# Kernel tuning notes

Hardware: AMD Instinct MI355X
Metric: run time of the kernel (lower is better)

The kernel has to match this reference:

```python
import jax, jax.numpy as jnp
import numpy as np

K = 1024   # codebook size
C = 8      # codebook channels
D = K // C # per-channel code dim = 128
BETA = 0.25
B = 8192   # batch of latent vectors, each of size C*D = K


def setup_inputs() -> dict:
    key = jax.random.key(0)
    k1, k2, k3 = jax.random.split(key, 3)
    latents = jax.random.normal(k1, (B, C * D), dtype=jnp.float32)
    # nn.Embedding(K, D) init: uniform(-1/K, 1/K)
    embedding = jax.random.uniform(k2, (K, D), dtype=jnp.float32,
                                   minval=-1.0 / K, maxval=1.0 / K)
    k = jax.random.randint(k3, (C,), 0, 8, dtype=jnp.int32)
    return {"latents": latents, "embedding": embedding, "k": k}


def reference(latents, embedding, k):
    sg = jax.lax.stop_gradient
    flat = latents.reshape(-1, D)                                  # [B*C, D]
    # squared euclidean distance to every code: [B*C, K]
    dist = (jnp.sum(flat ** 2, axis=1, keepdims=True)
            + jnp.sum(embedding ** 2, axis=1)
            - 2.0 * (flat @ embedding.T))
    order = jnp.argsort(dist, axis=1).reshape(-1, C, K)            # [B, C, K]
    # per channel c, pick the k[c]-th nearest code index
    sel = jnp.take_along_axis(order, k[None, :, None], axis=2)[..., 0]  # [B, C]
    # one-hot @ embedding == plain gather of selected rows
    quantized = embedding[sel.reshape(-1)].reshape(latents.shape)  # [B, C*D]
    commitment_loss = jnp.mean((sg(quantized) - latents) ** 2)
    embedding_loss = jnp.mean((quantized - sg(latents)) ** 2)
    vq_loss = BETA * commitment_loss + embedding_loss
    # straight-through estimator
    quantized_st = latents + sg(quantized - latents)
    return quantized_st, vq_loss
```

## Files before the change

### kernel.cpp

```cpp
#include <hip/hip_runtime.h>

#define KDIM   128
#define BM     128
#define NELEM  8388608

#define OFF_ESQ   36864
#define OFF_EBUF0 40960
#define OFF_FSQ   57344
#define OFF_SEL   57856
#define OFF_RED   58368
#define SMEM_SZ   58400

typedef __attribute__((ext_vector_type(8)))  short  short8;
typedef __attribute__((ext_vector_type(8)))  __bf16 bf16x8;
typedef __attribute__((ext_vector_type(4)))  float  f32x4;

__device__ inline ushort f2bf(float f) {
  unsigned u = __builtin_bit_cast(unsigned, f);
  u += 0x7fffu + ((u >> 16) & 1u);
  return (ushort)(u >> 16);
}
__device__ inline f32x4 mfma16(short8 a, short8 b, f32x4 c) {
  return __builtin_amdgcn_mfma_f32_16x16x32_bf16(
      __builtin_bit_cast(bf16x8, a), __builtin_bit_cast(bf16x8, b), c, 0, 0, 0);
}
__device__ inline void gload16(const void* g, void* l) {
  __builtin_amdgcn_global_load_lds(
      (const __attribute__((address_space(1))) unsigned*)g,
      (__attribute__((address_space(3))) unsigned*)l, 16, 0, 0);
}

__global__ void vq_prep(const float* __restrict__ emb, ushort* __restrict__ ebf,
                        float* __restrict__ esqm) {
  int j = blockIdx.x, d = threadIdx.x;
  float v = emb[j * KDIM + d];
  ebf[j * KDIM + (d ^ ((j & 7) << 3))] = f2bf(v);
  float s = v * v;
#pragma unroll
  for (int m = 1; m <= 32; m <<= 1) s += __shfl_xor(s, m);
  __shared__ float w[2];
  if ((threadIdx.x & 63) == 0) w[threadIdx.x >> 6] = s;
  __syncthreads();
  if (threadIdx.x == 0) esqm[j] = -0.5f * (w[0] + w[1]);
}

__global__ __launch_bounds__(256, 2) void vq_main(
    const float* __restrict__ lat, const float* __restrict__ emb,
    const int* __restrict__ ksel, const ushort* __restrict__ ebf,
    const float* __restrict__ esqm, float* __restrict__ out,
    float* __restrict__ partial) {
  __shared__ __align__(16) unsigned char smem[SMEM_SZ];
  ushort* fLds    = (ushort*)(smem);
  float*  mbuf    = (float*)(smem);
  float*  esqmLds = (float*)(smem + OFF_ESQ);
  float*  fsqLds  = (float*)(smem + OFF_FSQ);
  int*    selLds  = (int*)(smem + OFF_SEL);
  float*  redL    = (float*)(smem + OFF_RED);

  const int tid = threadIdx.x;
  const int lane = tid & 63, wid = tid >> 6;
  const int gR0 = blockIdx.x * BM;

  {
    const char* src = (const char*)ebf + tid * 16;
    char* dst = (char*)smem + OFF_EBUF0 + tid * 16;
#pragma unroll
    for (int q = 0; q < 4; ++q) gload16(src + q * 4096, dst + q * 4096);
  }
  ((float4*)esqmLds)[tid] = ((const float4*)esqm)[tid];

#pragma unroll
  for (int it = 0; it < 16; ++it) {
    int i = tid + it * 256;
    int row = i >> 5, c4 = i & 31;
    float4 v = *(const float4*)(lat + (size_t)(gR0 + row) * KDIM + c4 * 4);
    float s = v.x * v.x + v.y * v.y + v.z * v.z + v.w * v.w;
#pragma unroll
    for (int m = 1; m <= 16; m <<= 1) s += __shfl_xor(s, m);
    if ((i & 31) == 0) fsqLds[row] = s;
    ushort4 b; b.x = f2bf(v.x); b.y = f2bf(v.y); b.z = f2bf(v.z); b.w = f2bf(v.w);
    *(ushort4*)(&fLds[row * 144 + c4 * 4]) = b;
  }
  __syncthreads();

  const int n = lane & 15, hi = lane >> 4;
  const int g = wid >> 1, h = wid & 1;
  short8 bfr[4][4];
#pragma unroll
  for (int ct = 0; ct < 4; ++ct)
#pragma unroll
    for (int s = 0; s < 4; ++s)
      bfr[ct][s] = *(const short8*)(&fLds[(g * 64 + ct * 16 + n) * 144 + s * 32 + hi * 8]);
  asm volatile("s_waitcnt lgkmcnt(0)" ::: "memory");

  const int pb = ((hi ^ (n & 3)) << 4) | (((n >> 2) & 1) << 6);
  const int rowb = h * 8192 + n * 256;
  const char* aE0 = (const char*)smem + OFF_EBUF0 + rowb + pb;
  const char* aO0 = (const char*)smem + OFF_EBUF0 + rowb + (pb ^ 64);
  const char* aE1 = (const char*)smem + 0 + rowb + pb;
  const char* aO1 = (const char*)smem + 0 + rowb + (pb ^ 64);

  int cst[2][4];
#pragma unroll
  for (int t = 0; t < 2; ++t)
#pragma unroll
    for (int r = 0; r < 4; ++r) cst[t][r] = h * 32 + t * 16 + hi * 4 + r;

  const float NINF = __builtin_bit_cast(float, 0xFF800000u);
  float top[4][8];
#pragma unroll
  for (int ct = 0; ct < 4; ++ct)
#pragma unroll
    for (int p = 0; p < 8; ++p) top[ct][p] = NINF;

#pragma unroll 2
  for (int nn = 0; nn < 16; ++nn) {
    __builtin_amdgcn_s_barrier();
    if (nn < 15) {
      const char* src = (const char*)ebf + (nn + 1) * 16384 + tid * 16;
      char* dst = (char*)smem + ((nn & 1) ? OFF_EBUF0 : 0) + tid * 16;
#pragma unroll
      for (int q = 0; q < 4; ++q) gload16(src + q * 4096, dst + q * 4096);
      asm volatile("s_waitcnt vmcnt(4)" ::: "memory");
    } else {
      asm volatile("s_waitcnt vmcnt(0)" ::: "memory");
    }
    __builtin_amdgcn_s_barrier();

    const char* aEb = (nn & 1) ? aE1 : aE0;
    const char* aOb = (nn & 1) ? aO1 : aO0;

    f32x4 acc[2][4];
#pragma unroll
    for (int t = 0; t < 2; ++t) {
      f32x4 e = *(const f32x4*)(esqmLds + nn * 64 + h * 32 + t * 16 + hi * 4);
#pragma unroll
      for (int ct = 0; ct < 4; ++ct) acc[t][ct] = e;
    }
#pragma unroll
    for (int s = 0; s < 4; ++s) {
      const char* ab = (s & 1) ? aOb : aEb;
      const int so = (s >> 1) * 128;
      short8 a0 = *(const short8*)(ab + so);
      short8 a1 = *(const short8*)(ab + 4096 + so);
#pragma unroll
      for (int ct = 0; ct < 4; ++ct) {
        acc[0][ct] = mfma16(a0, bfr[ct][s], acc[0][ct]);
        acc[1][ct] = mfma16(a1, bfr[ct][s], acc[1][ct]);
      }
    }

#pragma unroll
    for (int ct = 0; ct < 4; ++ct) {
      float k[8];
#pragma unroll
      for (int t = 0; t < 2; ++t)
#pragma unroll
        for (int r = 0; r < 4; ++r) {
          unsigned bb = (__builtin_bit_cast(unsigned, acc[t][ct][r]) & 0xFFFFFC00u)
                        | (unsigned)cst[t][r];
          k[t * 4 + r] = __builtin_bit_cast(float, bb);
        }
      float x = fmaxf(fmaxf(k[0], k[1]), k[2]);
      float y = fmaxf(fmaxf(k[3], k[4]), k[5]);
      float c = fmaxf(fmaxf(x, y), fmaxf(k[6], k[7]));
      unsigned cb = __builtin_bit_cast(unsigned, c) | (unsigned)(nn << 6);
      float key = __builtin_bit_cast(float, cb);
#pragma unroll
      for (int p = 0; p < 8; ++p) {
        float mx = fmaxf(top[ct][p], key);
        key = fminf(top[ct][p], key);
        top[ct][p] = mx;
      }
    }
  }

  __syncthreads();

#pragma unroll
  for (int ct = 0; ct < 4; ++ct) {
    const int L = g * 64 + ct * 16 + n;
    const int sl = (h * 4 + hi) ^ (n & 7);
    float* dst = mbuf + L * 68 + sl * 8;
    *(f32x4*)(dst + 0) = (f32x4){top[ct][0], top[ct][1], top[ct][2], top[ct][3]};
    *(f32x4*)(dst + 4) = (f32x4){top[ct][4], top[ct][5], top[ct][6], top[ct][7]};
  }
  __syncthreads();

  if (tid < 128) {
    const int L = tid, xk = L & 7;
    int kk = ksel[L & 7]; kk = kk < 0 ? 0 : (kk > 7 ? 7 : kk);
    float hh[8]; int ix[8];
#pragma unroll
    for (int j = 0; j < 8; ++j) { hh[j] = mbuf[L * 68 + ((j ^ xk) << 3)]; ix[j] = 0; }
    float sel;
    for (int s = 0;; ++s) {
      float m01 = fmaxf(fmaxf(hh[0], hh[1]), fmaxf(hh[2], hh[3]));
      float m23 = fmaxf(fmaxf(hh[4], hh[5]), fmaxf(hh[6], hh[7]));
      sel = fmaxf(m01, m23);
      if (s == kk) break;
#pragma unroll
      for (int j = 0; j < 8; ++j) {
        if (hh[j] == sel) {
          ++ix[j];
          hh[j] = (ix[j] < 8) ? mbuf[L * 68 + ((j ^ xk) << 3) + ix[j]] : NINF;
        }
      }
    }
    unsigned sb = __builtin_bit_cast(unsigned, sel);
    selLds[L] = (int)(sb & 1023u);
    float val = __builtin_bit_cast(float, sb & 0xFFFFFC00u);
    float rl = fsqLds[L] - 2.0f * val;
#pragma unroll
    for (int m = 1; m <= 32; m <<= 1) rl += __shfl_xor(rl, m);
    if (lane == 0) redL[wid] = rl;
  }
  __syncthreads();
  if (tid == 0) partial[blockIdx.x] = redL[0] + redL[1];

#pragma unroll
  for (int it = 0; it < 16; ++it) {
    int i = tid + it * 256;
    int row = i >> 5, c4 = i & 31;
    int s2 = selLds[row];
    float4 q = *(const float4*)(emb + (size_t)s2 * KDIM + c4 * 4);
    *(float4*)(out + (size_t)(gR0 + row) * KDIM + c4 * 4) = q;
  }
}

__global__ void vq_reduce(const float* __restrict__ p, float* __restrict__ loss) {
  int t = threadIdx.x;
  double s = (double)p[t] + (double)p[t + 256];
#pragma unroll
  for (int m = 1; m <= 32; m <<= 1) s += __shfl_xor(s, m);
  __shared__ double w[4];
  if ((t & 63) == 0) w[t >> 6] = s;
  __syncthreads();
  if (t == 0) loss[0] = (float)((w[0] + w[1] + w[2] + w[3]) * (1.25 / 8388608.0));
}

extern "C" void kernel_launch(void* const* d_in, const int* in_sizes, int n_in,
                              void* d_out, int out_size, void* d_ws, size_t ws_size,
                              hipStream_t stream) {
  const float* lat = (const float*)d_in[0];
  const float* emb = (const float*)d_in[1];
  const int* ksel = (const int*)d_in[2];
  float* out = (float*)d_out;

  ushort* ebf = (ushort*)d_ws;
  float* esqm = (float*)((char*)d_ws + 262144);
  float* partial = (float*)((char*)d_ws + 266240);

  vq_prep<<<1024, 128, 0, stream>>>(emb, ebf, esqm);
  vq_main<<<512, 256, 0, stream>>>(lat, emb, ksel, ebf, esqm, out, partial);
  vq_reduce<<<1, 256, 0, stream>>>(partial, out + NELEM);
}
```

Measured before the change: 45.95 us.

## Restructure VQ main loop: per-wave rows, larger codebook chunks, register latent fragments

Each wave now owns 32 latent rows and scans the whole codebook, rather than two waves splitting columns for 64 rows. Latents are loaded straight from global memory into bf16 MFMA fragments, with no LDS staging pass. The codebook streams in 32KB double-buffered chunks over 8 iterations, with one barrier per chunk. Per-thread top-8 candidates now come from 4 column slots instead of 8, which shrinks the final merge. LDS use rises to about 70KB, which may reduce occupancy, and each codebook A fragment is reused across only 2 row tiles instead of 4.

```diff
diff --git a/kernel.cpp b/kernel.cpp
--- a/kernel.cpp
+++ b/kernel.cpp
@@ -1,15 +1,14 @@
 #include <hip/hip_runtime.h>
 
 #define KDIM   128
-#define BM     128
 #define NELEM  8388608
 
-#define OFF_ESQ   36864
-#define OFF_EBUF0 40960
-#define OFF_FSQ   57344
-#define OFF_SEL   57856
-#define OFF_RED   58368
-#define SMEM_SZ   58400
+#define OFF_EBUF 0
+#define OFF_ESQ  65536
+#define OFF_FSQ  69632
+#define OFF_SEL  70144
+#define OFF_RED  70656
+#define SMEM_SZ  70688
 
 typedef __attribute__((ext_vector_type(8)))  short  short8;
 typedef __attribute__((ext_vector_type(8)))  __bf16 bf16x8;
@@ -50,160 +49,156 @@
     const float* __restrict__ esqm, float* __restrict__ out,
     float* __restrict__ partial) {
   __shared__ __align__(16) unsigned char smem[SMEM_SZ];
-  ushort* fLds    = (ushort*)(smem);
-  float*  mbuf    = (float*)(smem);
-  float*  esqmLds = (float*)(smem + OFF_ESQ);
-  float*  fsqLds  = (float*)(smem + OFF_FSQ);
-  int*    selLds  = (int*)(smem + OFF_SEL);
-  float*  redL    = (float*)(smem + OFF_RED);
+  float* esqmLds = (float*)(smem + OFF_ESQ);
+  float* fsqLds  = (float*)(smem + OFF_FSQ);
+  int*   selLds  = (int*)(smem + OFF_SEL);
+  float* redL    = (float*)(smem + OFF_RED);
+  float* mbuf    = (float*)(smem + OFF_EBUF);
 
   const int tid = threadIdx.x;
   const int lane = tid & 63, wid = tid >> 6;
-  const int gR0 = blockIdx.x * BM;
+  const int gR0 = blockIdx.x * 128;
+  const int n = lane & 15, hi = lane >> 4;
 
   {
     const char* src = (const char*)ebf + tid * 16;
-    char* dst = (char*)smem + OFF_EBUF0 + tid * 16;
-#pragma unroll
-    for (int q = 0; q < 4; ++q) gload16(src + q * 4096, dst + q * 4096);
+    char* dst = (char*)smem + OFF_EBUF + tid * 16;
+#pragma unroll
+    for (int q = 0; q < 8; ++q) gload16(src + q * 4096, dst + q * 4096);
   }
   ((float4*)esqmLds)[tid] = ((const float4*)esqm)[tid];
 
-#pragma unroll
-  for (int it = 0; it < 16; ++it) {
-    int i = tid + it * 256;
-    int row = i >> 5, c4 = i & 31;
-    float4 v = *(const float4*)(lat + (size_t)(gR0 + row) * KDIM + c4 * 4);
-    float s = v.x * v.x + v.y * v.y + v.z * v.z + v.w * v.w;
-#pragma unroll
-    for (int m = 1; m <= 16; m <<= 1) s += __shfl_xor(s, m);
-    if ((i & 31) == 0) fsqLds[row] = s;
-    ushort4 b; b.x = f2bf(v.x); b.y = f2bf(v.y); b.z = f2bf(v.z); b.w = f2bf(v.w);
-    *(ushort4*)(&fLds[row * 144 + c4 * 4]) = b;
-  }
-  __syncthreads();
-
-  const int n = lane & 15, hi = lane >> 4;
-  const int g = wid >> 1, h = wid & 1;
-  short8 bfr[4][4];
-#pragma unroll
-  for (int ct = 0; ct < 4; ++ct)
-#pragma unroll
-    for (int s = 0; s < 4; ++s)
-      bfr[ct][s] = *(const short8*)(&fLds[(g * 64 + ct * 16 + n) * 144 + s * 32 + hi * 8]);
-  asm volatile("s_waitcnt lgkmcnt(0)" ::: "memory");
-
-  const int pb = ((hi ^ (n & 3)) << 4) | (((n >> 2) & 1) << 6);
-  const int rowb = h * 8192 + n * 256;
-  const char* aE0 = (const char*)smem + OFF_EBUF0 + rowb + pb;
-  const char* aO0 = (const char*)smem + OFF_EBUF0 + rowb + (pb ^ 64);
-  const char* aE1 = (const char*)smem + 0 + rowb + pb;
-  const char* aO1 = (const char*)smem + 0 + rowb + (pb ^ 64);
-
-  int cst[2][4];
-#pragma unroll
-  for (int t = 0; t < 2; ++t)
-#pragma unroll
-    for (int r = 0; r < 4; ++r) cst[t][r] = h * 32 + t * 16 + hi * 4 + r;
+  short8 bfr[2][4];
+  float fsqp[2];
+#pragma unroll
+  for (int ct = 0; ct < 2; ++ct) {
+    const float* rp = lat + (size_t)(gR0 + wid * 32 + ct * 16 + n) * KDIM + hi * 8;
+    float s = 0.f;
+#pragma unroll
+    for (int sfr = 0; sfr < 4; ++sfr) {
+      float4 v0 = *(const float4*)(rp + sfr * 32);
+      float4 v1 = *(const float4*)(rp + sfr * 32 + 4);
+      s += v0.x * v0.x + v0.y * v0.y + v0.z * v0.z + v0.w * v0.w
+         + v1.x * v1.x + v1.y * v1.y + v1.z * v1.z + v1.w * v1.w;
+      short8 b;
+      b[0] = (short)f2bf(v0.x); b[1] = (short)f2bf(v0.y);
+      b[2] = (short)f2bf(v0.z); b[3] = (short)f2bf(v0.w);
+      b[4] = (short)f2bf(v1.x); b[5] = (short)f2bf(v1.y);
+      b[6] = (short)f2bf(v1.z); b[7] = (short)f2bf(v1.w);
+      bfr[ct][sfr] = b;
+    }
+    fsqp[ct] = s;
+  }
+#pragma unroll
+  for (int ct = 0; ct < 2; ++ct) {
+    float s = fsqp[ct];
+    s += __shfl_xor(s, 16);
+    s += __shfl_xor(s, 32);
+    if (hi == 0) fsqLds[wid * 32 + ct * 16 + n] = s;
+  }
+  asm volatile("s_waitcnt vmcnt(0)" ::: "memory");
+  __syncthreads();
+
+  const int nm = n & 7;
+  const int pb = ((hi ^ (nm & 3)) << 4) | (((nm >> 2) & 1) << 6);
+  const char* aE0 = (const char*)smem + OFF_EBUF + n * 256 + pb;
+  const char* aO0 = (const char*)smem + OFF_EBUF + n * 256 + (pb ^ 64);
+
+  int cidx[4];
+#pragma unroll
+  for (int r = 0; r < 4; ++r) cidx[r] = hi * 4 + r;
 
   const float NINF = __builtin_bit_cast(float, 0xFF800000u);
-  float top[4][8];
-#pragma unroll
-  for (int ct = 0; ct < 4; ++ct)
+  float top[2][8];
+#pragma unroll
+  for (int ct = 0; ct < 2; ++ct)
 #pragma unroll
     for (int p = 0; p < 8; ++p) top[ct][p] = NINF;
+  float kq[2][4];
 
 #pragma unroll 2
-  for (int nn = 0; nn < 16; ++nn) {
-    __builtin_amdgcn_s_barrier();
-    if (nn < 15) {
-      const char* src = (const char*)ebf + (nn + 1) * 16384 + tid * 16;
-      char* dst = (char*)smem + ((nn & 1) ? OFF_EBUF0 : 0) + tid * 16;
-#pragma unroll
-      for (int q = 0; q < 4; ++q) gload16(src + q * 4096, dst + q * 4096);
-      asm volatile("s_waitcnt vmcnt(4)" ::: "memory");
-    } else {
+  for (int nn = 0; nn < 8; ++nn) {
+    const int cb = (nn & 1) * 32768;
+    if (nn < 7) {
+      const char* src = (const char*)ebf + (nn + 1) * 32768 + tid * 16;
+      char* dst = (char*)smem + OFF_EBUF + (((nn + 1) & 1) * 32768) + tid * 16;
+#pragma unroll
+      for (int q = 0; q < 8; ++q) gload16(src + q * 4096, dst + q * 4096);
+    }
+    const float* eqb = esqmLds + nn * 128 + hi * 4;
+#pragma unroll
+    for (int tp = 0; tp < 8; ++tp) {
+      f32x4 e = *(const f32x4*)(eqb + tp * 16);
+      f32x4 acc0 = e, acc1 = e;
+#pragma unroll
+      for (int s = 0; s < 4; ++s) {
+        const char* ab = ((s & 1) ? aO0 : aE0) + cb + tp * 4096 + (s >> 1) * 128;
+        short8 a = *(const short8*)ab;
+        acc0 = mfma16(a, bfr[0][s], acc0);
+        acc1 = mfma16(a, bfr[1][s], acc1);
+      }
+      float kn[2][4];
+#pragma unroll
+      for (int r = 0; r < 4; ++r) {
+        kn[0][r] = __builtin_bit_cast(float,
+            (__builtin_bit_cast(unsigned, acc0[r]) & 0xFFFFFC00u) | (unsigned)cidx[r]);
+        kn[1][r] = __builtin_bit_cast(float,
+            (__builtin_bit_cast(unsigned, acc1[r]) & 0xFFFFFC00u) | (unsigned)cidx[r]);
+        cidx[r] += 16;
+      }
+      if ((tp & 1) == 0) {
+#pragma unroll
+        for (int ct = 0; ct < 2; ++ct)
+#pragma unroll
+          for (int r = 0; r < 4; ++r) kq[ct][r] = kn[ct][r];
+      } else {
+#pragma unroll
+        for (int ct = 0; ct < 2; ++ct) {
+          float x = fmaxf(fmaxf(kq[ct][0], kq[ct][1]), fmaxf(kq[ct][2], kq[ct][3]));
+          float y = fmaxf(fmaxf(kn[ct][0], kn[ct][1]), fmaxf(kn[ct][2], kn[ct][3]));
+          float key = fmaxf(x, y);
+#pragma unroll
+          for (int p = 0; p < 8; ++p) {
+            float mx = fmaxf(top[ct][p], key);
+            key = fminf(top[ct][p], key);
+            top[ct][p] = mx;
+          }
+        }
+      }
+    }
+    if (nn < 7) {
       asm volatile("s_waitcnt vmcnt(0)" ::: "memory");
-    }
-    __builtin_amdgcn_s_barrier();
-
-    const char* aEb = (nn & 1) ? aE1 : aE0;
-    const char* aOb = (nn & 1) ? aO1 : aO0;
-
-    f32x4 acc[2][4];
-#pragma unroll
-    for (int t = 0; t < 2; ++t) {
-      f32x4 e = *(const f32x4*)(esqmLds + nn * 64 + h * 32 + t * 16 + hi * 4);
-#pragma unroll
-      for (int ct = 0; ct < 4; ++ct) acc[t][ct] = e;
-    }
-#pragma unroll
-    for (int s = 0; s < 4; ++s) {
-      const char* ab = (s & 1) ? aOb : aEb;
-      const int so = (s >> 1) * 128;
-      short8 a0 = *(const short8*)(ab + so);
-      short8 a1 = *(const short8*)(ab + 4096 + so);
-#pragma unroll
-      for (int ct = 0; ct < 4; ++ct) {
-        acc[0][ct] = mfma16(a0, bfr[ct][s], acc[0][ct]);
-        acc[1][ct] = mfma16(a1, bfr[ct][s], acc[1][ct]);
-      }
-    }
-
-#pragma unroll
-    for (int ct = 0; ct < 4; ++ct) {
-      float k[8];
-#pragma unroll
-      for (int t = 0; t < 2; ++t)
-#pragma unroll
-        for (int r = 0; r < 4; ++r) {
-          unsigned bb = (__builtin_bit_cast(unsigned, acc[t][ct][r]) & 0xFFFFFC00u)
-                        | (unsigned)cst[t][r];
-          k[t * 4 + r] = __builtin_bit_cast(float, bb);
-        }
-      float x = fmaxf(fmaxf(k[0], k[1]), k[2]);
-      float y = fmaxf(fmaxf(k[3], k[4]), k[5]);
-      float c = fmaxf(fmaxf(x, y), fmaxf(k[6], k[7]));
-      unsigned cb = __builtin_bit_cast(unsigned, c) | (unsigned)(nn << 6);
-      float key = __builtin_bit_cast(float, cb);
-#pragma unroll
-      for (int p = 0; p < 8; ++p) {
-        float mx = fmaxf(top[ct][p], key);
-        key = fminf(top[ct][p], key);
-        top[ct][p] = mx;
-      }
-    }
-  }
-
-  __syncthreads();
-
-#pragma unroll
-  for (int ct = 0; ct < 4; ++ct) {
-    const int L = g * 64 + ct * 16 + n;
-    const int sl = (h * 4 + hi) ^ (n & 7);
-    float* dst = mbuf + L * 68 + sl * 8;
+      __builtin_amdgcn_s_barrier();
+    }
+  }
+
+  __syncthreads();
+
+#pragma unroll
+  for (int ct = 0; ct < 2; ++ct) {
+    const int L = wid * 32 + ct * 16 + n;
+    const int sl = hi ^ (n & 3);
+    float* dst = mbuf + L * 36 + sl * 8;
     *(f32x4*)(dst + 0) = (f32x4){top[ct][0], top[ct][1], top[ct][2], top[ct][3]};
     *(f32x4*)(dst + 4) = (f32x4){top[ct][4], top[ct][5], top[ct][6], top[ct][7]};
   }
   __syncthreads();
 
   if (tid < 128) {
-    const int L = tid, xk = L & 7;
+    const int L = tid, xk = L & 3;
     int kk = ksel[L & 7]; kk = kk < 0 ? 0 : (kk > 7 ? 7 : kk);
-    float hh[8]; int ix[8];
-#pragma unroll
-    for (int j = 0; j < 8; ++j) { hh[j] = mbuf[L * 68 + ((j ^ xk) << 3)]; ix[j] = 0; }
+    float hh[4]; int ix[4];
+#pragma unroll
+    for (int j = 0; j < 4; ++j) { hh[j] = mbuf[L * 36 + ((j ^ xk) << 3)]; ix[j] = 0; }
     float sel;
     for (int s = 0;; ++s) {
-      float m01 = fmaxf(fmaxf(hh[0], hh[1]), fmaxf(hh[2], hh[3]));
-      float m23 = fmaxf(fmaxf(hh[4], hh[5]), fmaxf(hh[6], hh[7]));
-      sel = fmaxf(m01, m23);
+      sel = fmaxf(fmaxf(hh[0], hh[1]), fmaxf(hh[2], hh[3]));
       if (s == kk) break;
 #pragma unroll
-      for (int j = 0; j < 8; ++j) {
+      for (int j = 0; j < 4; ++j) {
         if (hh[j] == sel) {
           ++ix[j];
-          hh[j] = (ix[j] < 8) ? mbuf[L * 68 + ((j ^ xk) << 3) + ix[j]] : NINF;
+          hh[j] = (ix[j] < 8) ? mbuf[L * 36 + ((j ^ xk) << 3) + ix[j]] : NINF;
         }
       }
     }
```

Measured after the change: 44.53 us. 1.03x faster.
